# Kernel optimization log

Measured on AMD Instinct MI355X. Metric: run time of the kernel, lower is better.

## Reference

```python
import jax, jax.numpy as jnp
import numpy as np

PI = float(np.pi)
EPS = 1e-7


def conv2d(x, w, b, pad=0):
    y = jax.lax.conv_general_dilated(x, w, (1, 1), [(pad, pad), (pad, pad)],
                                     dimension_numbers=('NCHW', 'OIHW', 'NCHW'))
    return y + b[None, :, None, None]


def nearest_resize(x, oh, ow):
    # PyTorch F.interpolate(mode='nearest'): src_idx = floor(dst_idx * in/out)
    ih, iw = x.shape[-2], x.shape[-1]
    ri = (jnp.arange(oh) * ih) // oh
    ci = (jnp.arange(ow) * iw) // ow
    return x[:, :, ri, :][:, :, :, ci]


def maxpool_to(x, oh, ow):
    # adaptive_max_pool2d with divisible sizes == strided max pool
    b, c, h, w = x.shape
    return x.reshape(b, c, oh, h // oh, ow, w // ow).max(axis=(3, 5))


def minmax(t):
    # per-sample min-max normalization over (channel,h,w)
    mn = t.min(axis=(1, 2, 3), keepdims=True)
    mx = t.max(axis=(1, 2, 3), keepdims=True)
    return (t - mn) / (mx - mn + EPS)


def nonlocal2d(x, g_w, g_b, th_w, th_b, ph_w, ph_b, out_w, out_b):
    # embedded-Gaussian NonLocal2D, reduction=1, use_scale=False
    b, c, h, w = x.shape
    g_x = conv2d(x, g_w, g_b).reshape(b, c, h * w).transpose(0, 2, 1)    # (b, hw, c)
    th = conv2d(x, th_w, th_b).reshape(b, c, h * w).transpose(0, 2, 1)   # (b, hw, c)
    ph = conv2d(x, ph_w, ph_b).reshape(b, c, h * w)                      # (b, c, hw)
    pw = jax.nn.softmax(jnp.einsum('bic,bcj->bij', th, ph), axis=-1)     # (b, hw, hw)
    y = jnp.einsum('bij,bjc->bic', pw, g_x).transpose(0, 2, 1).reshape(b, c, h, w)
    return x + conv2d(y, out_w, out_b)


def reference(x0, x1, x2, x3, x4, rc_w, rc_b,
              nl_g_w, nl_g_b, nl_theta_w, nl_theta_b,
              nl_phi_w, nl_phi_b, nl_out_w, nl_out_b):
    inputs = [x0, x1, x2, x3, x4]
    refine_level = 2
    gh, gw = inputs[refine_level].shape[2:]
    feats = []
    for i, x in enumerate(inputs):
        if i < refine_level:
            feats.append(maxpool_to(x, gh, gw))
        else:
            feats.append(nearest_resize(x, gh, gw))
    ori_fe = sum(feats) / len(feats)
    bsf = nonlocal2d(ori_fe, nl_g_w, nl_g_b, nl_theta_w, nl_theta_b,
                     nl_phi_w, nl_phi_b, nl_out_w, nl_out_b)

    outs = []
    for i, x in enumerate(inputs):
        b, c, h, w = x.shape
        # ConvModule(C->1, 3x3, relu) then extra F.relu (idempotent)
        basic_map = jax.nn.relu(conv2d(x, rc_w[i], rc_b[i], pad=1))      # (b,1,h,w)
        row = x.mean(axis=3)[:, 0, :]                                     # (b,h)
        col = x.mean(axis=2)[:, 0, :]                                     # (b,w)
        avg_map = minmax((row[:, :, None] * col[:, None, :])[:, None])    # (b,1,h,w)
        basic_reg = minmax(basic_map)
        distance_map = jnp.cos((avg_map - basic_reg) * (PI / 2))
        attention = jax.nn.relu(nearest_resize(bsf, h, w) * distance_map)
        outs.append(x + attention)
    return tuple(outs)


def setup_inputs() -> dict:
    key = jax.random.key(0)
    ks = jax.random.split(key, 16)
    C = 256
    sizes = [200, 100, 50, 25, 13]
    inp = {}
    for i, s in enumerate(sizes):
        inp[f'x{i}'] = jax.random.normal(ks[i], (4, C, s, s), dtype=jnp.float32)
    inp['rc_w'] = jax.random.normal(ks[5], (5, 1, C, 3, 3), dtype=jnp.float32) * 0.02
    inp['rc_b'] = jnp.zeros((5, 1), dtype=jnp.float32)
    inp['nl_g_w'] = jax.random.normal(ks[6], (C, C, 1, 1), dtype=jnp.float32) * 0.02
    inp['nl_g_b'] = jnp.zeros((C,), dtype=jnp.float32)
    inp['nl_theta_w'] = jax.random.normal(ks[7], (C, C, 1, 1), dtype=jnp.float32) * 0.02
    inp['nl_theta_b'] = jnp.zeros((C,), dtype=jnp.float32)
    inp['nl_phi_w'] = jax.random.normal(ks[8], (C, C, 1, 1), dtype=jnp.float32) * 0.02
    inp['nl_phi_b'] = jnp.zeros((C,), dtype=jnp.float32)
    inp['nl_out_w'] = jax.random.normal(ks[9], (C, C, 1, 1), dtype=jnp.float32) * 0.02
    inp['nl_out_b'] = jnp.zeros((C,), dtype=jnp.float32)
    return inp
```

## Files before the change

kernel.cpp:

```cpp
#include <hip/hip_runtime.h>
#include <math.h>

typedef __attribute__((ext_vector_type(8))) short short8;
typedef __attribute__((ext_vector_type(4))) float f32x4;
typedef __attribute__((ext_vector_type(4))) unsigned short u16x4;

#define EPSV 1e-7f
#define PI_2 1.57079632679489662f
#define NEG_BIG (-3.4e38f)

constexpr int B = 4, C = 256;
constexpr int GW = 50;
constexpr int PR = 2500, PP = 2560;
constexpr int CPP = C * PP;
constexpr long long SPB = (long long)PP * PP;
constexpr int PS = PP * C;
constexpr int ZT = 213176;

constexpr size_t OFF_ORI   = 0;
constexpr size_t OFF_BSF   = OFF_ORI + (size_t)B * CPP;
constexpr size_t OFF_Z     = OFF_BSF + (size_t)B * CPP;
constexpr size_t OFF_BASIC = OFF_Z + (size_t)9 * ZT;
constexpr size_t OFF_ROW   = OFF_BASIC + 213184;
constexpr size_t OFF_COL   = OFF_ROW + 1600;
constexpr size_t OFF_STATS = OFF_COL + 1600;
constexpr size_t OFF_RSUM  = OFF_STATS + 128;
constexpr size_t OFF_U16   = OFF_RSUM + 10240;
constexpr size_t U_ORIT = 0;
constexpr size_t U_THT  = U_ORIT + (size_t)B * CPP;
constexpr size_t U_PHT  = U_THT  + (size_t)B * CPP;
constexpr size_t U_G    = U_PHT  + (size_t)B * CPP;
constexpr size_t U_YTT  = U_G    + (size_t)B * CPP;
constexpr size_t U_WB   = U_YTT  + (size_t)B * CPP;

__device__ __forceinline__ unsigned short f2b(float x) {
    union { float f; unsigned u; } q{x};
    unsigned r = q.u + 0x7FFFu + ((q.u >> 16) & 1u);
    return (unsigned short)(r >> 16);
}
__device__ __forceinline__ float b2f(unsigned short u) {
    union { unsigned u; float f; } q{(unsigned)u << 16};
    return q.f;
}

__device__ __forceinline__ float orife_val(
    int idx, const float* __restrict__ x0, const float* __restrict__ x1,
    const float* __restrict__ x2, const float* __restrict__ x3,
    const float* __restrict__ x4)
{
    int p = idx % PP; int bc = idx / PP;
    if (p >= PR) return 0.0f;
    int y = p / GW, x = p % GW;
    const float* p0 = x0 + (size_t)bc * 40000;
    float m0 = NEG_BIG;
    #pragma unroll
    for (int dy = 0; dy < 4; dy++) {
        f32x4 r = *(const f32x4*)(p0 + (y * 4 + dy) * 200 + x * 4);
        m0 = fmaxf(m0, fmaxf(fmaxf(r[0], r[1]), fmaxf(r[2], r[3])));
    }
    const float* p1 = x1 + (size_t)bc * 10000;
    float m1 = fmaxf(fmaxf(p1[(y*2)*100 + x*2],   p1[(y*2)*100 + x*2+1]),
                     fmaxf(p1[(y*2+1)*100 + x*2], p1[(y*2+1)*100 + x*2+1]));
    float v2 = x2[(size_t)bc * 2500 + p];
    float v3 = x3[(size_t)bc * 625 + (y/2)*25 + (x/2)];
    int ry = (y * 13) / 50, rx = (x * 13) / 50;
    float v4 = x4[(size_t)bc * 169 + ry * 13 + rx];
    return (m0 + m1 + v2 + v3 + v4) * 0.2f;
}

constexpr int ORIFE_T = 2560 * 256;

__global__ __launch_bounds__(256) void k_pre(
    const float* __restrict__ x0, const float* __restrict__ x1,
    const float* __restrict__ x2, const float* __restrict__ x3,
    const float* __restrict__ x4, const float* __restrict__ rc_w,
    const float* __restrict__ wth, const float* __restrict__ wph,
    const float* __restrict__ wg,  const float* __restrict__ wout,
    unsigned short* __restrict__ wb, float* __restrict__ ori,
    float* __restrict__ z, float* __restrict__ row, float* __restrict__ col,
    float* __restrict__ rowsum)
{
    __shared__ float wsm[C * 12];
    const int bx = blockIdx.x;
    const int tid = threadIdx.x;

    if (bx < 388) {
        int rid = bx * 4 + (tid >> 6);
        int lane = tid & 63;
        int base, H; const float* x;
        if      (rid < 800)  { base = 0;    H = 200; x = x0; }
        else if (rid < 1200) { base = 800;  H = 100; x = x1; }
        else if (rid < 1400) { base = 1200; H = 50;  x = x2; }
        else if (rid < 1500) { base = 1400; H = 25;  x = x3; }
        else                 { base = 1500; H = 13;  x = x4; }
        int r = rid - base; int b = r / H, h = r - (r / H) * H;
        const float* xr = x + (size_t)b * C * H * H + (size_t)h * H;
        float s = 0.0f;
        for (int w = lane; w < H; w += 64) s += xr[w];
        #pragma unroll
        for (int off = 32; off > 0; off >>= 1) s += __shfl_down(s, off);
        if (lane == 0) row[rid] = s / (float)H;
    } else if (bx < 395) {
        int idx = (bx - 388) * 256 + tid;
        if (idx >= 1552) return;
        int base, H; const float* x;
        if      (idx < 800)  { base = 0;    H = 200; x = x0; }
        else if (idx < 1200) { base = 800;  H = 100; x = x1; }
        else if (idx < 1400) { base = 1200; H = 50;  x = x2; }
        else if (idx < 1500) { base = 1400; H = 25;  x = x3; }
        else                 { base = 1500; H = 13;  x = x4; }
        int r = idx - base; int b = r / H, w = r - (r / H) * H;
        const float* xc = x + (size_t)b * C * H * H + w;
        float s = 0.0f;
        int h = 0;
        for (; h + 3 < H; h += 4) {
            float a0 = xc[(size_t)h * H];
            float a1 = xc[(size_t)(h + 1) * H];
            float a2 = xc[(size_t)(h + 2) * H];
            float a3 = xc[(size_t)(h + 3) * H];
            s += (a0 + a1) + (a2 + a3);
        }
        for (; h < H; h++) s += xc[(size_t)h * H];
        col[idx] = s / (float)H;
    } else if (bx < 1419) {
        int idx = (bx - 395) * 256 + tid;
        int seg = idx >> 16, off = idx & 65535;
        const float* s = (seg == 0) ? wth : (seg == 1) ? wph : (seg == 2) ? wg : wout;
        wb[idx] = f2b(s[off]);
    } else if (bx < 2254) {
        int bxx = bx - 1419;
        int lvl, base, HW, zb; const float* x;
        if      (bxx < 625) { lvl = 0; base = 0;   HW = 40000; zb = 0;      x = x0; }
        else if (bxx < 782) { lvl = 1; base = 625; HW = 10000; zb = 160000; x = x1; }
        else if (bxx < 822) { lvl = 2; base = 782; HW = 2500;  zb = 200000; x = x2; }
        else if (bxx < 832) { lvl = 3; base = 822; HW = 625;   zb = 210000; x = x3; }
        else                { lvl = 4; base = 832; HW = 169;   zb = 212500; x = x4; }

        const float* w9 = rc_w + (size_t)lvl * C * 9;
        for (int i = tid; i < C * 9; i += 256) wsm[(i / 9) * 12 + (i % 9)] = w9[i];
        __syncthreads();

        int idx = (bxx - base) * 256 + tid;
        if (idx >= B * HW) return;
        int b = idx / HW, p = idx - b * HW;

        float acc[9] = {};
        const float* xp = x + (size_t)b * C * HW + p;
        for (int c0 = 0; c0 < C; c0 += 8) {
            float v[8];
            #pragma unroll
            for (int k = 0; k < 8; k++) v[k] = xp[(size_t)(c0 + k) * HW];
            #pragma unroll
            for (int k = 0; k < 8; k++) {
                const float* wc = &wsm[(c0 + k) * 12];
                f32x4 w0 = *(const f32x4*)wc;
                f32x4 w1 = *(const f32x4*)(wc + 4);
                float w8 = wc[8];
                acc[0] += v[k] * w0[0]; acc[1] += v[k] * w0[1];
                acc[2] += v[k] * w0[2]; acc[3] += v[k] * w0[3];
                acc[4] += v[k] * w1[0]; acc[5] += v[k] * w1[1];
                acc[6] += v[k] * w1[2]; acc[7] += v[k] * w1[3];
                acc[8] += v[k] * w8;
            }
        }
        #pragma unroll
        for (int t = 0; t < 9; t++)
            z[(size_t)t * ZT + zb + idx] = acc[t];
    } else if (bx < 4814) {
        int t0 = (bx - 2254) * 256 + tid;
        #pragma unroll
        for (int k = 0; k < 4; k++) {
            int idx = t0 + k * ORIFE_T;
            ori[idx] = orife_val(idx, x0, x1, x2, x3, x4);
        }
    } else {
        int idx = (bx - 4814) * 1024 + tid * 4;
        f32x4 zv = {0.0f, 0.0f, 0.0f, 0.0f};
        *(f32x4*)(rowsum + idx) = zv;
    }
}

__global__ __launch_bounds__(256) void k_tcvt(const float* __restrict__ ori,
                                              unsigned short* __restrict__ ot)
{
    __shared__ unsigned short t[64][66];
    int p0 = blockIdx.x * 64, c0 = blockIdx.y * 64, b = blockIdx.z;
    int pp = threadIdx.x & 63, cb = threadIdx.x >> 6;
    #pragma unroll
    for (int i = 0; i < 16; i++) {
        int cc = cb * 16 + i;
        t[cc][pp] = f2b(ori[((size_t)b * C + c0 + cc) * PP + p0 + pp]);
    }
    __syncthreads();
    int cc2 = threadIdx.x & 63, pb = threadIdx.x >> 6;
    #pragma unroll
    for (int i = 0; i < 16; i++) {
        int pp2 = pb * 16 + i;
        ot[((size_t)b * PP + p0 + pp2) * C + c0 + cc2] = t[cc2][pp2];
    }
}

constexpr int LDT = 40;

__global__ __launch_bounds__(256) void k_proj(
    const unsigned short* __restrict__ wb, const unsigned short* __restrict__ orit,
    const float* __restrict__ th_b, const float* __restrict__ ph_b,
    const float* __restrict__ g_b,
    unsigned short* __restrict__ tht, unsigned short* __restrict__ pht,
    unsigned short* __restrict__ gb)
{
    __shared__ __align__(16) unsigned short As[128 * LDT];
    __shared__ __align__(16) unsigned short Bs[128 * LDT];

    const int z = blockIdx.z;
    const int b = z / 3, wsel = z - b * 3;
    const bool tp = (wsel < 2);
    const unsigned short* A = tp ? (orit + (size_t)b * CPP) : (wb + 131072);
    const unsigned short* Bm = tp ? (wb + wsel * 65536) : (orit + (size_t)b * CPP);
    const float* bias = (wsel == 0) ? th_b : (wsel == 1) ? ph_b : g_b;

    const int m0 = (tp ? blockIdx.x : blockIdx.y) * 128;
    const int n0 = (tp ? blockIdx.y : blockIdx.x) * 128;
    const int tid = threadIdx.x;
    const int lane = tid & 63, w = tid >> 6;
    const int wm = (w & 1) * 64, wn = (w >> 1) * 64;
    const int fr = lane & 15, fq = lane >> 4;

    f32x4 acc[4][4] = {};
    for (int k0 = 0; k0 < 256; k0 += 32) {
        #pragma unroll
        for (int l = 0; l < 2; l++) {
            int li = tid + l * 256;
            int rr = li >> 2, kc = li & 3;
            short8 va = *(const short8*)(A  + (size_t)(m0 + rr) * 256 + k0 + kc * 8);
            short8 vb = *(const short8*)(Bm + (size_t)(n0 + rr) * 256 + k0 + kc * 8);
            *(short8*)&As[rr * LDT + kc * 8] = va;
            *(short8*)&Bs[rr * LDT + kc * 8] = vb;
        }
        __syncthreads();
        short8 af[4], bf[4];
        #pragma unroll
        for (int i = 0; i < 4; i++)
            af[i] = *(const short8*)&As[(wm + i * 16 + fr) * LDT + fq * 8];
        #pragma unroll
        for (int j = 0; j < 4; j++)
            bf[j] = *(const short8*)&Bs[(wn + j * 16 + fr) * LDT + fq * 8];
        #pragma unroll
        for (int i = 0; i < 4; i++)
            #pragma unroll
            for (int j = 0; j < 4; j++)
                acc[i][j] = __builtin_amdgcn_mfma_f32_16x16x32_bf16(
                    af[i], bf[j], acc[i][j], 0, 0, 0);
        __syncthreads();
    }

    unsigned short* dst = (wsel == 0) ? tht : (wsel == 1) ? pht : gb;
    dst += (size_t)b * CPP;
    #pragma unroll
    for (int i = 0; i < 4; i++) {
        #pragma unroll
        for (int r = 0; r < 4; r++) {
            int gm = m0 + wm + i * 16 + fq * 4 + r;
            #pragma unroll
            for (int j = 0; j < 4; j++) {
                int gn = n0 + wn + j * 16 + fr;
                float v = acc[i][j][r] + (tp ? bias[gn] : bias[gm]);
                if (!tp && gn >= PR) v = 0.0f;
                size_t off = tp ? ((size_t)gm * 256 + gn) : ((size_t)gm * PP + gn);
                dst[off] = f2b(v);
            }
        }
    }
}

template<bool AddBias, bool AddRes, bool OutBf, bool AExp>
__global__ __launch_bounds__(256) void k_bgemm(
    const unsigned short* __restrict__ A, const unsigned short* __restrict__ Bm,
    const float* __restrict__ bias, const float* __restrict__ res,
    void* __restrict__ Cout, int K, int lda, int ldb, int ldc,
    long long sA, long long sB, long long sC, long long sR,
    int nsplit, long long sK, float* __restrict__ rowsum)
{
    __shared__ __align__(16) unsigned short As[128 * LDT];
    __shared__ __align__(16) unsigned short Bs[128 * LDT];

    const int z = blockIdx.z;
    const int bz = z / nsplit, ks = z - bz * nsplit;
    A  += (size_t)sA * bz + (size_t)sK * ks;
    Bm += (size_t)sB * bz + (size_t)sK * ks;
    const long long kofs = (long long)sK * ks;

    const int m0 = blockIdx.y * 128, n0 = blockIdx.x * 128;
    const int tid = threadIdx.x;
    const int lane = tid & 63, w = tid >> 6;
    const int wm = (w & 1) * 64, wn = (w >> 1) * 64;
    const int fr = lane & 15, fq = lane >> 4;

    const bool dosum = AExp && (blockIdx.x == 0);
    float rs[2] = {0.0f, 0.0f};

    f32x4 acc[4][4] = {};
    for (int k0 = 0; k0 < K; k0 += 32) {
        #pragma unroll
        for (int l = 0; l < 2; l++) {
            int li = tid + l * 256;
            int rr = li >> 2, kc = li & 3;
            short8 va = *(const short8*)(A  + (size_t)(m0 + rr) * lda + k0 + kc * 8);
            if constexpr (AExp) {
                long long cb = kofs + k0 + kc * 8;
                float ssum = 0.0f;
                #pragma unroll
                for (int e = 0; e < 8; e++) {
                    float f = __expf(b2f((unsigned short)va[e]));
                    if (cb + e < PR) ssum += f;
                    va[e] = (short)f2b(f);
                }
                if (dosum) rs[l] += ssum;
            }
            short8 vb = *(const short8*)(Bm + (size_t)(n0 + rr) * ldb + k0 + kc * 8);
            *(short8*)&As[rr * LDT + kc * 8] = va;
            *(short8*)&Bs[rr * LDT + kc * 8] = vb;
        }
        __syncthreads();
        short8 af[4], bf[4];
        #pragma unroll
        for (int i = 0; i < 4; i++)
            af[i] = *(const short8*)&As[(wm + i * 16 + fr) * LDT + fq * 8];
        #pragma unroll
        for (int j = 0; j < 4; j++)
            bf[j] = *(const short8*)&Bs[(wn + j * 16 + fr) * LDT + fq * 8];
        #pragma unroll
        for (int i = 0; i < 4; i++)
            #pragma unroll
            for (int j = 0; j < 4; j++)
                acc[i][j] = __builtin_amdgcn_mfma_f32_16x16x32_bf16(
                    af[i], bf[j], acc[i][j], 0, 0, 0);
        __syncthreads();
    }

    if constexpr (AExp) {
        if (dosum) {
            #pragma unroll
            for (int l = 0; l < 2; l++) {
                float s = rs[l];
                s += __shfl_xor(s, 1);
                s += __shfl_xor(s, 2);
                if ((tid & 3) == 0) {
                    int row = (tid >> 2) + l * 64;
                    atomicAdd(&rowsum[(size_t)bz * PP + m0 + row], s);
                }
            }
        }
    }

    float* Cf = (float*)Cout;
    unsigned short* Cb = (unsigned short*)Cout;
    const size_t co = (size_t)sC * z;
    const size_t ro = (size_t)sR * bz;
    #pragma unroll
    for (int i = 0; i < 4; i++) {
        #pragma unroll
        for (int r = 0; r < 4; r++) {
            int gm = m0 + wm + i * 16 + fq * 4 + r;
            #pragma unroll
            for (int j = 0; j < 4; j++) {
                int gn = n0 + wn + j * 16 + fr;
                float v = acc[i][j][r];
                if (AddBias) v += bias[gm];
                if (AddRes)  v += res[ro + (size_t)gm * ldc + gn];
                size_t off = co + (size_t)gm * ldc + gn;
                if (OutBf) Cb[off] = f2b(v);
                else       Cf[off] = v;
            }
        }
    }
}

__global__ __launch_bounds__(256) void k_ytred(const float* __restrict__ part,
                                               const float* __restrict__ rowsum,
                                               unsigned short* __restrict__ ytt)
{
    int idx = blockIdx.x * 256 + threadIdx.x;
    if (idx >= B * CPP / 4) return;
    int b = idx / (CPP / 4);
    int r = idx - b * (CPP / 4);
    const float* p = part + (size_t)(b * 2) * PS + (size_t)r * 4;
    f32x4 s = *(const f32x4*)p;
    f32x4 q = *(const f32x4*)(p + PS);
    int p_row = r >> 6;
    float inv = 1.0f / rowsum[(size_t)b * PP + p_row];
    u16x4 o;
    #pragma unroll
    for (int k = 0; k < 4; k++) o[k] = f2b((s[k] + q[k]) * inv);
    *(u16x4*)(ytt + (size_t)b * CPP + (size_t)r * 4) = o;
}

template<int H, int ZB>
__device__ __forceinline__ void ccomb_impl(int idx, const float* __restrict__ z,
                                           float biasv, float* __restrict__ bas)
{
    constexpr int W = H, HW = H * W;
    int r = idx - ZB; int b = r / HW; int p = r - b * HW;
    int y = p / W, x = p - (p / W) * W;
    float acc = biasv;
    #pragma unroll
    for (int dy = 0; dy < 3; dy++) {
        int yy = y + dy - 1;
        if (yy < 0 || yy >= H) continue;
        #pragma unroll
        for (int dx = 0; dx < 3; dx++) {
            int xx = x + dx - 1;
            if (xx < 0 || xx >= W) continue;
            acc += z[(size_t)(dy * 3 + dx) * ZT + ZB + (size_t)b * HW + yy * W + xx];
        }
    }
    bas[idx] = fmaxf(acc, 0.0f);
}

__global__ __launch_bounds__(256) void k_ccomb_f(const float* __restrict__ z,
                                                 const float* __restrict__ rb,
                                                 float* __restrict__ bas)
{
    int idx = blockIdx.x * 256 + threadIdx.x;
    if (idx >= ZT) return;
    if      (idx < 160000) ccomb_impl<200, 0>     (idx, z, rb[0], bas);
    else if (idx < 200000) ccomb_impl<100, 160000>(idx, z, rb[1], bas);
    else if (idx < 210000) ccomb_impl<50,  200000>(idx, z, rb[2], bas);
    else if (idx < 212500) ccomb_impl<25,  210000>(idx, z, rb[3], bas);
    else                   ccomb_impl<13,  212500>(idx, z, rb[4], bas);
}

__global__ __launch_bounds__(256) void k_stats_f(
    const float* __restrict__ row, const float* __restrict__ col,
    const float* __restrict__ basic, float* __restrict__ stats)
{
    const int Ht[5]  = {200, 100, 50, 25, 13};
    const int ZBt[5] = {0, 160000, 200000, 210000, 212500};
    const int RBt[5] = {0, 800, 1200, 1400, 1500};
    int lvl = blockIdx.x >> 2, b = blockIdx.x & 3;
    int H = Ht[lvl], HW = H * H;
    const float* rw = row + RBt[lvl] + b * H;
    const float* cl = col + RBt[lvl] + b * H;
    const float* bb = basic + ZBt[lvl] + (size_t)b * HW;

    __shared__ float smn[256], smx[256];
    int t = threadIdx.x;
    float rmn, rmx, cmn, cmx, bmn, bmx;

    float mn = 3.4e38f, mx = NEG_BIG;
    for (int h = t; h < H; h += 256) { float v = rw[h]; mn = fminf(mn, v); mx = fmaxf(mx, v); }
    smn[t] = mn; smx[t] = mx; __syncthreads();
    for (int s = 128; s > 0; s >>= 1) { if (t < s) { smn[t] = fminf(smn[t], smn[t+s]); smx[t] = fmaxf(smx[t], smx[t+s]); } __syncthreads(); }
    rmn = smn[0]; rmx = smx[0]; __syncthreads();

    mn = 3.4e38f; mx = NEG_BIG;
    for (int w = t; w < H; w += 256) { float v = cl[w]; mn = fminf(mn, v); mx = fmaxf(mx, v); }
    smn[t] = mn; smx[t] = mx; __syncthreads();
    for (int s = 128; s > 0; s >>= 1) { if (t < s) { smn[t] = fminf(smn[t], smn[t+s]); smx[t] = fmaxf(smx[t], smx[t+s]); } __syncthreads(); }
    cmn = smn[0]; cmx = smx[0]; __syncthreads();

    mn = 3.4e38f; mx = NEG_BIG;
    for (int i = t; i < HW; i += 256) { float v = bb[i]; mn = fminf(mn, v); mx = fmaxf(mx, v); }
    smn[t] = mn; smx[t] = mx; __syncthreads();
    for (int s = 128; s > 0; s >>= 1) { if (t < s) { smn[t] = fminf(smn[t], smn[t+s]); smx[t] = fmaxf(smx[t], smx[t+s]); } __syncthreads(); }
    bmn = smn[0]; bmx = smx[0];

    if (t == 0) {
        float p1 = rmn * cmn, p2 = rmn * cmx, p3 = rmx * cmn, p4 = rmx * cmx;
        float amn = fminf(fminf(p1, p2), fminf(p3, p4));
        float amx = fmaxf(fmaxf(p1, p2), fmaxf(p3, p4));
        float* st = stats + lvl * 16 + b * 4;
        st[0] = amn; st[1] = amx; st[2] = bmn; st[3] = bmx;
    }
}

template<int H, int ZB, int RB, int LVL>
__device__ __forceinline__ void dist_impl(int idx, float* __restrict__ basic,
                                          const float* __restrict__ row,
                                          const float* __restrict__ col,
                                          const float* __restrict__ stats)
{
    constexpr int HW = H * H;
    int r = idx - ZB; int b = r / HW; int p = r - b * HW;
    int yh = p / H, xw = p - (p / H) * H;
    const float* st = stats + LVL * 16 + b * 4;
    float amn = st[0], amx = st[1], bmn = st[2], bmx = st[3];
    float an = (row[RB + b * H + yh] * col[RB + b * H + xw] - amn) / (amx - amn + EPSV);
    float bn = (basic[idx] - bmn) / (bmx - bmn + EPSV);
    basic[idx] = cosf((an - bn) * PI_2);
}

__global__ __launch_bounds__(256) void k_dist_f(float* __restrict__ basic,
                                                const float* __restrict__ row,
                                                const float* __restrict__ col,
                                                const float* __restrict__ stats)
{
    int idx = blockIdx.x * 256 + threadIdx.x;
    if (idx >= ZT) return;
    if      (idx < 160000) dist_impl<200, 0,      0,    0>(idx, basic, row, col, stats);
    else if (idx < 200000) dist_impl<100, 160000, 800,  1>(idx, basic, row, col, stats);
    else if (idx < 210000) dist_impl<50,  200000, 1200, 2>(idx, basic, row, col, stats);
    else if (idx < 212500) dist_impl<25,  210000, 1400, 3>(idx, basic, row, col, stats);
    else                   dist_impl<13,  212500, 1500, 4>(idx, basic, row, col, stats);
}

template<int LVL>
__device__ __forceinline__ void final_v4(int vid, const float* __restrict__ x,
                                         const unsigned short* __restrict__ bsf,
                                         const float* __restrict__ dist,
                                         float* __restrict__ out)
{
    constexpr int H = (LVL == 0) ? 200 : 100;
    constexpr int W = H, HW = H * W, Wv = W / 4;
    int xv = vid % Wv; int t = vid / Wv;
    int yh = t % H; t /= H; int c = t % C; int b = t / C;
    f32x4 xw4 = *(const f32x4*)(x + (size_t)vid * 4);
    f32x4 d4  = *(const f32x4*)(dist + (size_t)b * HW + yh * W + xv * 4);
    const unsigned short* bb = bsf + ((size_t)b * C + c) * PP;
    f32x4 o;
    if constexpr (LVL == 0) {
        float bv = b2f(bb[(yh >> 2) * GW + xv]);
        #pragma unroll
        for (int k = 0; k < 4; k++) o[k] = xw4[k] + fmaxf(bv * d4[k], 0.0f);
    } else {
        float bv0 = b2f(bb[(yh >> 1) * GW + 2 * xv]);
        float bv1 = b2f(bb[(yh >> 1) * GW + 2 * xv + 1]);
        o[0] = xw4[0] + fmaxf(bv0 * d4[0], 0.0f);
        o[1] = xw4[1] + fmaxf(bv0 * d4[1], 0.0f);
        o[2] = xw4[2] + fmaxf(bv1 * d4[2], 0.0f);
        o[3] = xw4[3] + fmaxf(bv1 * d4[3], 0.0f);
    }
    *(f32x4*)(out + (size_t)vid * 4) = o;
}

template<int LVL>
__device__ __forceinline__ void final_s(int idx, const float* __restrict__ x,
                                        const unsigned short* __restrict__ bsf,
                                        const float* __restrict__ dist,
                                        float* __restrict__ out)
{
    constexpr int H = (LVL == 2) ? 50 : (LVL == 3) ? 25 : 13;
    constexpr int W = H, HW = H * W;
    int xw = idx % W; int t = idx / W;
    int yh = t % H; t /= H; int c = t % C; int b = t / C;
    float d = dist[(size_t)b * HW + yh * W + xw];
    constexpr bool ident = (LVL == 2);
    int ry = ident ? yh : (yh * GW) / H;
    int rx = ident ? xw : (xw * GW) / W;
    float bv = b2f(bsf[((size_t)b * C + c) * PP + ry * GW + rx]);
    out[idx] = x[idx] + fmaxf(bv * d, 0.0f);
}

__global__ __launch_bounds__(256) void k_final_f(
    const float* __restrict__ x0, const float* __restrict__ x1,
    const float* __restrict__ x2, const float* __restrict__ x3,
    const float* __restrict__ x4, const unsigned short* __restrict__ bsf,
    const float* __restrict__ basic, float* __restrict__ out)
{
    int bx = blockIdx.x;
    int tid = threadIdx.x;
    if (bx < 8000) {
        int t0 = bx * 256 + tid;
        #pragma unroll
        for (int k = 0; k < 5; k++)
            final_v4<0>(t0 + k * 2048000, x0, bsf, basic, out);
    } else if (bx < 10000) {
        int t0 = (bx - 8000) * 256 + tid;
        #pragma unroll
        for (int k = 0; k < 5; k++)
            final_v4<1>(t0 + k * 512000, x1, bsf, basic + 160000, out + 40960000ull);
    } else if (bx < 12000) {
        int t0 = (bx - 10000) * 256 + tid;
        #pragma unroll
        for (int k = 0; k < 5; k++)
            final_s<2>(t0 + k * 512000, x2, bsf, basic + 200000, out + 51200000ull);
    } else if (bx < 12500) {
        int t0 = (bx - 12000) * 256 + tid;
        #pragma unroll
        for (int k = 0; k < 5; k++)
            final_s<3>(t0 + k * 128000, x3, bsf, basic + 210000, out + 53760000ull);
    } else {
        int t0 = (bx - 12500) * 256 + tid;
        #pragma unroll
        for (int k = 0; k < 4; k++)
            final_s<4>(t0 + k * 43264, x4, bsf, basic + 212500, out + 54400000ull);
    }
}

extern "C" void kernel_launch(void* const* d_in, const int* in_sizes, int n_in,
                              void* d_out, int out_size, void* d_ws, size_t ws_size,
                              hipStream_t stream)
{
    const float* x[5]; for (int i = 0; i < 5; i++) x[i] = (const float*)d_in[i];
    const float* rc_w  = (const float*)d_in[5];
    const float* rc_b  = (const float*)d_in[6];
    const float* g_b   = (const float*)d_in[8];
    const float* th_b  = (const float*)d_in[10];
    const float* ph_b  = (const float*)d_in[12];
    const float* out_b = (const float*)d_in[14];
    float* out = (float*)d_out;

    float* ws    = (float*)d_ws;
    float* ori   = ws + OFF_ORI;
    unsigned short* bsf = (unsigned short*)(ws + OFF_BSF);
    float* zbuf  = ws + OFF_Z;
    float* basic = ws + OFF_BASIC;
    float* rowb  = ws + OFF_ROW;
    float* colb  = ws + OFF_COL;
    float* stats = ws + OFF_STATS;
    float* rowsum = ws + OFF_RSUM;
    unsigned short* u16 = (unsigned short*)(ws + OFF_U16);
    unsigned short* orit = u16 + U_ORIT;
    unsigned short* tht  = u16 + U_THT;
    unsigned short* pht  = u16 + U_PHT;
    unsigned short* gb   = u16 + U_G;
    unsigned short* ytt  = u16 + U_YTT;
    unsigned short* wb   = u16 + U_WB;
    unsigned short* wb_out = wb + 196608;

    unsigned short* S_all = (unsigned short*)out;
    float* part = out + 4 * SPB;

    k_pre<<<4824, 256, 0, stream>>>(
        x[0], x[1], x[2], x[3], x[4], rc_w,
        (const float*)d_in[9], (const float*)d_in[11],
        (const float*)d_in[7], (const float*)d_in[13],
        wb, ori, zbuf, rowb, colb, rowsum);

    k_tcvt<<<dim3(PP / 64, C / 64, B), 256, 0, stream>>>(ori, orit);

    k_proj<<<dim3(20, 2, 12), 256, 0, stream>>>(wb, orit, th_b, ph_b, g_b, tht, pht, gb);

    k_ccomb_f<<<(ZT + 255) / 256, 256, 0, stream>>>(zbuf, rc_b, basic);
    k_stats_f<<<20, 256, 0, stream>>>(rowb, colb, basic, stats);
    k_dist_f<<<(ZT + 255) / 256, 256, 0, stream>>>(basic, rowb, colb, stats);

    dim3 gsc(PP / 128, PP / 128, B);
    k_bgemm<false, false, true, false><<<gsc, 256, 0, stream>>>(
        tht, pht, nullptr, nullptr, S_all, C, C, C, PP, CPP, CPP, SPB, 0, 1, 0, nullptr);

    dim3 gyt(C / 128, PP / 128, B * 2);
    k_bgemm<false, false, false, true><<<gyt, 256, 0, stream>>>(
        S_all, gb, nullptr, nullptr, part, PP / 2, PP, PP, C, SPB, CPP, PS, 0, 2, PP / 2,
        rowsum);

    k_ytred<<<(B * CPP / 4 + 255) / 256, 256, 0, stream>>>(part, rowsum, ytt);

    dim3 gbsf(PP / 128, C / 128, B);
    k_bgemm<true, true, true, false><<<gbsf, 256, 0, stream>>>(
        wb_out, ytt, out_b, ori, bsf, C, C, C, PP, 0, CPP, CPP, CPP, 1, 0, nullptr);

    k_final_f<<<12669, 256, 0, stream>>>(
        x[0], x[1], x[2], x[3], x[4], bsf, basic, out);
}
```

Baseline: 334.9 us.

## Fuse softmax exp into score GEMM epilogue and fold y reduction into out-proj

The exp and row-sum of the attention softmax move from the A-load path of the P·G GEMM (previously recomputed per N-tile) into the epilogue of the score GEMM, which now writes exp values and atomically accumulates row sums. The separate k_ytred kernel is removed: the output-projection GEMM reads the two fp32 split-K partials directly, sums and normalizes them while loading B tiles. The 3x3 reduction conv prep also processes two pixels per thread with paired loads and stores, halving its block count. This drops one launch and an intermediate bf16 buffer at the cost of wider fp32 B loads in the last GEMM and more atomics in the score GEMM.

```diff
diff --git a/kernel.cpp b/kernel.cpp
--- a/kernel.cpp
+++ b/kernel.cpp
@@ -3,6 +3,7 @@
 
 typedef __attribute__((ext_vector_type(8))) short short8;
 typedef __attribute__((ext_vector_type(4))) float f32x4;
+typedef __attribute__((ext_vector_type(2))) float f32x2;
 typedef __attribute__((ext_vector_type(4))) unsigned short u16x4;
 
 #define EPSV 1e-7f
@@ -127,54 +128,67 @@
         int seg = idx >> 16, off = idx & 65535;
         const float* s = (seg == 0) ? wth : (seg == 1) ? wph : (seg == 2) ? wg : wout;
         wb[idx] = f2b(s[off]);
-    } else if (bx < 2254) {
+    } else if (bx < 1838) {
         int bxx = bx - 1419;
-        int lvl, base, HW, zb; const float* x;
-        if      (bxx < 625) { lvl = 0; base = 0;   HW = 40000; zb = 0;      x = x0; }
-        else if (bxx < 782) { lvl = 1; base = 625; HW = 10000; zb = 160000; x = x1; }
-        else if (bxx < 822) { lvl = 2; base = 782; HW = 2500;  zb = 200000; x = x2; }
-        else if (bxx < 832) { lvl = 3; base = 822; HW = 625;   zb = 210000; x = x3; }
-        else                { lvl = 4; base = 832; HW = 169;   zb = 212500; x = x4; }
+        int lvl, base, HW, PH, zb; const float* x;
+        if      (bxx < 313) { lvl = 0; base = 0;   HW = 40000; PH = 20000; zb = 0;      x = x0; }
+        else if (bxx < 392) { lvl = 1; base = 313; HW = 10000; PH = 5000;  zb = 160000; x = x1; }
+        else if (bxx < 412) { lvl = 2; base = 392; HW = 2500;  PH = 1250;  zb = 200000; x = x2; }
+        else if (bxx < 417) { lvl = 3; base = 412; HW = 625;   PH = 313;   zb = 210000; x = x3; }
+        else                { lvl = 4; base = 417; HW = 169;   PH = 85;    zb = 212500; x = x4; }
+        const bool alig = (HW & 1) == 0;
 
         const float* w9 = rc_w + (size_t)lvl * C * 9;
         for (int i = tid; i < C * 9; i += 256) wsm[(i / 9) * 12 + (i % 9)] = w9[i];
         __syncthreads();
 
         int idx = (bxx - base) * 256 + tid;
-        if (idx >= B * HW) return;
-        int b = idx / HW, p = idx - b * HW;
-
-        float acc[9] = {};
-        const float* xp = x + (size_t)b * C * HW + p;
+        if (idx >= B * PH) return;
+        int b = idx / PH, pp = (idx - b * PH) * 2;
+        bool has2 = (pp + 1 < HW);
+
+        float acc0[9] = {}, acc1[9] = {};
+        const float* xp = x + (size_t)b * C * HW + pp;
         for (int c0 = 0; c0 < C; c0 += 8) {
-            float v[8];
+            float v0[8], v1[8];
             #pragma unroll
-            for (int k = 0; k < 8; k++) v[k] = xp[(size_t)(c0 + k) * HW];
+            for (int k = 0; k < 8; k++) {
+                const float* a = xp + (size_t)(c0 + k) * HW;
+                if (alig && has2) { f32x2 t = *(const f32x2*)a; v0[k] = t[0]; v1[k] = t[1]; }
+                else { v0[k] = a[0]; v1[k] = has2 ? a[1] : 0.0f; }
+            }
             #pragma unroll
             for (int k = 0; k < 8; k++) {
                 const float* wc = &wsm[(c0 + k) * 12];
                 f32x4 w0 = *(const f32x4*)wc;
                 f32x4 w1 = *(const f32x4*)(wc + 4);
                 float w8 = wc[8];
-                acc[0] += v[k] * w0[0]; acc[1] += v[k] * w0[1];
-                acc[2] += v[k] * w0[2]; acc[3] += v[k] * w0[3];
-                acc[4] += v[k] * w1[0]; acc[5] += v[k] * w1[1];
-                acc[6] += v[k] * w1[2]; acc[7] += v[k] * w1[3];
-                acc[8] += v[k] * w8;
+                acc0[0] += v0[k] * w0[0]; acc1[0] += v1[k] * w0[0];
+                acc0[1] += v0[k] * w0[1]; acc1[1] += v1[k] * w0[1];
+                acc0[2] += v0[k] * w0[2]; acc1[2] += v1[k] * w0[2];
+                acc0[3] += v0[k] * w0[3]; acc1[3] += v1[k] * w0[3];
+                acc0[4] += v0[k] * w1[0]; acc1[4] += v1[k] * w1[0];
+                acc0[5] += v0[k] * w1[1]; acc1[5] += v1[k] * w1[1];
+                acc0[6] += v0[k] * w1[2]; acc1[6] += v1[k] * w1[2];
+                acc0[7] += v0[k] * w1[3]; acc1[7] += v1[k] * w1[3];
+                acc0[8] += v0[k] * w8;    acc1[8] += v1[k] * w8;
             }
         }
         #pragma unroll
-        for (int t = 0; t < 9; t++)
-            z[(size_t)t * ZT + zb + idx] = acc[t];
-    } else if (bx < 4814) {
-        int t0 = (bx - 2254) * 256 + tid;
+        for (int t = 0; t < 9; t++) {
+            size_t o = (size_t)t * ZT + zb + (size_t)b * HW + pp;
+            if (alig && has2) { f32x2 wv = {acc0[t], acc1[t]}; *(f32x2*)&z[o] = wv; }
+            else { z[o] = acc0[t]; if (has2) z[o + 1] = acc1[t]; }
+        }
+    } else if (bx < 4398) {
+        int t0 = (bx - 1838) * 256 + tid;
         #pragma unroll
         for (int k = 0; k < 4; k++) {
             int idx = t0 + k * ORIFE_T;
             ori[idx] = orife_val(idx, x0, x1, x2, x3, x4);
         }
     } else {
-        int idx = (bx - 4814) * 1024 + tid * 4;
+        int idx = (bx - 4398) * 1024 + tid * 4;
         f32x4 zv = {0.0f, 0.0f, 0.0f, 0.0f};
         *(f32x4*)(rowsum + idx) = zv;
     }
@@ -273,13 +287,14 @@
     }
 }
 
-template<bool AddBias, bool AddRes, bool OutBf, bool AExp>
+template<bool AddBias, bool AddRes, bool OutBf, bool OutExp, bool BParts>
 __global__ __launch_bounds__(256) void k_bgemm(
     const unsigned short* __restrict__ A, const unsigned short* __restrict__ Bm,
     const float* __restrict__ bias, const float* __restrict__ res,
     void* __restrict__ Cout, int K, int lda, int ldb, int ldc,
     long long sA, long long sB, long long sC, long long sR,
-    int nsplit, long long sK, float* __restrict__ rowsum)
+    int nsplit, long long sK,
+    float* __restrict__ rowsum, const float* __restrict__ parts)
 {
     __shared__ __align__(16) unsigned short As[128 * LDT];
     __shared__ __align__(16) unsigned short Bs[128 * LDT];
@@ -288,7 +303,6 @@
     const int bz = z / nsplit, ks = z - bz * nsplit;
     A  += (size_t)sA * bz + (size_t)sK * ks;
     Bm += (size_t)sB * bz + (size_t)sK * ks;
-    const long long kofs = (long long)sK * ks;
 
     const int m0 = blockIdx.y * 128, n0 = blockIdx.x * 128;
     const int tid = threadIdx.x;
@@ -296,8 +310,13 @@
     const int wm = (w & 1) * 64, wn = (w >> 1) * 64;
     const int fr = lane & 15, fq = lane >> 4;
 
-    const bool dosum = AExp && (blockIdx.x == 0);
-    float rs[2] = {0.0f, 0.0f};
+    float inv0 = 0.0f, inv1 = 0.0f;
+    const float* pbase = nullptr;
+    if constexpr (BParts) {
+        pbase = parts + (size_t)(bz * 2) * PS;
+        inv0 = 1.0f / rowsum[(size_t)bz * PP + n0 + (tid >> 2)];
+        inv1 = 1.0f / rowsum[(size_t)bz * PP + n0 + ((tid + 256) >> 2)];
+    }
 
     f32x4 acc[4][4] = {};
     for (int k0 = 0; k0 < K; k0 += 32) {
@@ -305,19 +324,23 @@
         for (int l = 0; l < 2; l++) {
             int li = tid + l * 256;
             int rr = li >> 2, kc = li & 3;
-            short8 va = *(const short8*)(A  + (size_t)(m0 + rr) * lda + k0 + kc * 8);
-            if constexpr (AExp) {
-                long long cb = kofs + k0 + kc * 8;
-                float ssum = 0.0f;
+            short8 va = *(const short8*)(A + (size_t)(m0 + rr) * lda + k0 + kc * 8);
+            short8 vb;
+            if constexpr (BParts) {
+                const float* pb = pbase + (size_t)(n0 + rr) * 256 + k0 + kc * 8;
+                f32x4 a0 = *(const f32x4*)pb;
+                f32x4 a1 = *(const f32x4*)(pb + 4);
+                f32x4 b0 = *(const f32x4*)(pb + PS);
+                f32x4 b1 = *(const f32x4*)(pb + PS + 4);
+                float inv = l ? inv1 : inv0;
                 #pragma unroll
-                for (int e = 0; e < 8; e++) {
-                    float f = __expf(b2f((unsigned short)va[e]));
-                    if (cb + e < PR) ssum += f;
-                    va[e] = (short)f2b(f);
+                for (int e = 0; e < 4; e++) {
+                    vb[e]     = (short)f2b((a0[e] + b0[e]) * inv);
+                    vb[e + 4] = (short)f2b((a1[e] + b1[e]) * inv);
                 }
-                if (dosum) rs[l] += ssum;
+            } else {
+                vb = *(const short8*)(Bm + (size_t)(n0 + rr) * ldb + k0 + kc * 8);
             }
-            short8 vb = *(const short8*)(Bm + (size_t)(n0 + rr) * ldb + k0 + kc * 8);
             *(short8*)&As[rr * LDT + kc * 8] = va;
             *(short8*)&Bs[rr * LDT + kc * 8] = vb;
         }
@@ -338,25 +361,11 @@
         __syncthreads();
     }
 
-    if constexpr (AExp) {
-        if (dosum) {
-            #pragma unroll
-            for (int l = 0; l < 2; l++) {
-                float s = rs[l];
-                s += __shfl_xor(s, 1);
-                s += __shfl_xor(s, 2);
-                if ((tid & 3) == 0) {
-                    int row = (tid >> 2) + l * 64;
-                    atomicAdd(&rowsum[(size_t)bz * PP + m0 + row], s);
-                }
-            }
-        }
-    }
-
     float* Cf = (float*)Cout;
     unsigned short* Cb = (unsigned short*)Cout;
     const size_t co = (size_t)sC * z;
     const size_t ro = (size_t)sR * bz;
+    float rsacc[4][4] = {};
     #pragma unroll
     for (int i = 0; i < 4; i++) {
         #pragma unroll
@@ -366,33 +375,35 @@
             for (int j = 0; j < 4; j++) {
                 int gn = n0 + wn + j * 16 + fr;
                 float v = acc[i][j][r];
-                if (AddBias) v += bias[gm];
-                if (AddRes)  v += res[ro + (size_t)gm * ldc + gn];
+                if constexpr (AddBias) v += bias[gm];
+                if constexpr (AddRes)  v += res[ro + (size_t)gm * ldc + gn];
                 size_t off = co + (size_t)gm * ldc + gn;
-                if (OutBf) Cb[off] = f2b(v);
-                else       Cf[off] = v;
+                if constexpr (OutExp) {
+                    float e = (gn < PR) ? __expf(v) : 0.0f;
+                    Cb[off] = f2b(e);
+                    rsacc[i][r] += e;
+                } else if constexpr (OutBf) {
+                    Cb[off] = f2b(v);
+                } else {
+                    Cf[off] = v;
+                }
             }
         }
     }
-}
-
-__global__ __launch_bounds__(256) void k_ytred(const float* __restrict__ part,
-                                               const float* __restrict__ rowsum,
-                                               unsigned short* __restrict__ ytt)
-{
-    int idx = blockIdx.x * 256 + threadIdx.x;
-    if (idx >= B * CPP / 4) return;
-    int b = idx / (CPP / 4);
-    int r = idx - b * (CPP / 4);
-    const float* p = part + (size_t)(b * 2) * PS + (size_t)r * 4;
-    f32x4 s = *(const f32x4*)p;
-    f32x4 q = *(const f32x4*)(p + PS);
-    int p_row = r >> 6;
-    float inv = 1.0f / rowsum[(size_t)b * PP + p_row];
-    u16x4 o;
-    #pragma unroll
-    for (int k = 0; k < 4; k++) o[k] = f2b((s[k] + q[k]) * inv);
-    *(u16x4*)(ytt + (size_t)b * CPP + (size_t)r * 4) = o;
+    if constexpr (OutExp) {
+        #pragma unroll
+        for (int i = 0; i < 4; i++)
+            #pragma unroll
+            for (int r = 0; r < 4; r++) {
+                float s = rsacc[i][r];
+                s += __shfl_xor(s, 1);
+                s += __shfl_xor(s, 2);
+                s += __shfl_xor(s, 4);
+                s += __shfl_xor(s, 8);
+                if (fr == 0)
+                    atomicAdd(&rowsum[(size_t)bz * PP + m0 + wm + i * 16 + fq * 4 + r], s);
+            }
+    }
 }
 
 template<int H, int ZB>
@@ -614,14 +625,13 @@
     unsigned short* tht  = u16 + U_THT;
     unsigned short* pht  = u16 + U_PHT;
     unsigned short* gb   = u16 + U_G;
-    unsigned short* ytt  = u16 + U_YTT;
     unsigned short* wb   = u16 + U_WB;
     unsigned short* wb_out = wb + 196608;
 
-    unsigned short* S_all = (unsigned short*)out;
+    unsigned short* P_all = (unsigned short*)out;
     float* part = out + 4 * SPB;
 
-    k_pre<<<4824, 256, 0, stream>>>(
+    k_pre<<<4408, 256, 0, stream>>>(
         x[0], x[1], x[2], x[3], x[4], rc_w,
         (const float*)d_in[9], (const float*)d_in[11],
         (const float*)d_in[7], (const float*)d_in[13],
@@ -636,19 +646,19 @@
     k_dist_f<<<(ZT + 255) / 256, 256, 0, stream>>>(basic, rowb, colb, stats);
 
     dim3 gsc(PP / 128, PP / 128, B);
-    k_bgemm<false, false, true, false><<<gsc, 256, 0, stream>>>(
-        tht, pht, nullptr, nullptr, S_all, C, C, C, PP, CPP, CPP, SPB, 0, 1, 0, nullptr);
+    k_bgemm<false, false, false, true, false><<<gsc, 256, 0, stream>>>(
+        tht, pht, nullptr, nullptr, P_all, C, C, C, PP, CPP, CPP, SPB, 0, 1, 0,
+        rowsum, nullptr);
 
     dim3 gyt(C / 128, PP / 128, B * 2);
-    k_bgemm<false, false, false, true><<<gyt, 256, 0, stream>>>(
-        S_all, gb, nullptr, nullptr, part, PP / 2, PP, PP, C, SPB, CPP, PS, 0, 2, PP / 2,
-        rowsum);
-
-    k_ytred<<<(B * CPP / 4 + 255) / 256, 256, 0, stream>>>(part, rowsum, ytt);
+    k_bgemm<false, false, false, false, false><<<gyt, 256, 0, stream>>>(
+        P_all, gb, nullptr, nullptr, part, PP / 2, PP, PP, C, SPB, CPP, PS, 0, 2, PP / 2,
+        nullptr, nullptr);
 
     dim3 gbsf(PP / 128, C / 128, B);
-    k_bgemm<true, true, true, false><<<gbsf, 256, 0, stream>>>(
-        wb_out, ytt, out_b, ori, bsf, C, C, C, PP, 0, CPP, CPP, CPP, 1, 0, nullptr);
+    k_bgemm<true, true, true, false, true><<<gbsf, 256, 0, stream>>>(
+        wb_out, (const unsigned short*)part, out_b, ori, bsf, C, C, 0, PP,
+        0, 0, CPP, CPP, 1, 0, rowsum, part);
 
     k_final_f<<<12669, 256, 0, stream>>>(
         x[0], x[1], x[2], x[3], x[4], bsf, basic, out);
```

Result: slower. 375.6 us (+12.2%).
